# Kernel tuning notes

Measured on AMD Instinct MI355X. Metric: run time of the kernel, lower is better.

Reference implementation:

```python
import jax, jax.numpy as jnp
import numpy as np

# --- configuration constants (match init_kwargs) ---
N = 256          # num_oscillators
T = 200          # simulation steps
INTERVAL = 5     # readout_update_interval
OFFSET = 1       # spike_update_offset
DELAY = 10
D = DELAY + 1    # delay-buffer length
K_GLOBAL = 1.0   # global_coupling_strength
STEP_SIZE = 0.1
GAMMA_ATTR = 0.5 # gamma_attraction_strength
DECAY = 0.9      # membrane_decay
THRESH = 1.0
REC_SCALE = 0.1
ALPHA_FIX = 0.5  # fixed_alpha_value (fixed during training)
CLS_START = 50   # classifier_start_step
SURR_BETA = 4.0  # surrogate-gradient sharpness
NUM_CLASSES = 10


def _spike(u):
    # Heaviside forward, sigmoid surrogate backward (straight-through)
    sg = jax.nn.sigmoid(SURR_BETA * u)
    hard = (u > 0).astype(u.dtype)
    return sg + jax.lax.stop_gradient(hard - sg)


def _forward(x, theta0, W_init, omega, W_ro, W_gate, W_rec, W_fb, W_cls, b_cls):
    B = x.shape[0]
    P = W_gate.shape[1]  # num_pixels = H*W*C
    xf = x.reshape(B, -1)
    gamma0 = jnp.tanh(xf @ W_init)                 # ReadoutLayer.initialize_gamma_from_input -> [B,N]
    buf0 = jnp.tile(theta0[None], (D, 1, 1))       # theta delay buffer [D,B,N]
    zN = jnp.zeros((B, N), x.dtype)
    zP = jnp.zeros((B, P), x.dtype)
    carry0 = (theta0, gamma0, zN, zP, zP, zN, buf0)  # theta, gamma, gate, membrane, spikes, fb-activity a, buffer

    def step(carry, s):
        theta, gamma, gate, mem, spk, a, buf = carry
        # --- KuramotoLayer: dtheta_i = omega_i + K/N * sum_j (1 + W_ij*alpha) sin(th_j - th_i) + attr*gamma_i
        # top-down connectivity W_ij = a_i a_j is rank-1, so the coupling sum is computed exactly in O(N).
        sin_t = jnp.sin(theta); cos_t = jnp.cos(theta)
        S = sin_t.sum(-1, keepdims=True); C = cos_t.sum(-1, keepdims=True)
        base = cos_t * S - sin_t * C
        as_ = jnp.sum(a * sin_t, -1, keepdims=True)
        ac_ = jnp.sum(a * cos_t, -1, keepdims=True)
        weighted = ALPHA_FIX * (cos_t * a * as_ - sin_t * a * ac_)
        dtheta = omega + (K_GLOBAL / N) * (base + weighted) + GAMMA_ATTR * gamma
        theta = theta + STEP_SIZE * dtheta

        # --- ReadoutLayer.gamma_update + SinusoidalGate every INTERVAL steps
        def ro_upd(args):
            g = jnp.tanh(theta @ W_ro)
            gt = g * 0.5 * (1.0 + jnp.cos(theta - buf[0]))  # gate from delayed phase difference
            return g, gt
        gamma, gate = jax.lax.cond((s % INTERVAL) == 0, ro_upd, lambda args: args, (gamma, gate))

        # --- SNNLayer.forward_step + TopDownFeedback on offset spike-update steps
        def sp_upd(args):
            mem_, spk_, a_ = args
            cur = gate @ W_gate + REC_SCALE * (spk_ @ W_rec)
            mem_ = DECAY * mem_ * (1.0 - spk_) + cur       # leaky membrane with reset
            spk_ = _spike(mem_ - THRESH)
            a_ = jnp.tanh(spk_ @ W_fb)                     # per-oscillator feedback activity
            return mem_, spk_, a_
        m_sp = (((s - OFFSET) % INTERVAL) == 0) & (s > OFFSET)
        mem, spk, a = jax.lax.cond(m_sp, sp_upd, lambda args: args, (mem, spk, a))

        buf = jnp.concatenate([buf[1:], theta[None]], axis=0)
        return (theta, gamma, gate, mem, spk, a, buf), spk

    _, spk_hist = jax.lax.scan(step, carry0, jnp.arange(1, T + 1))
    spike_trace = jnp.transpose(spk_hist, (1, 0, 2))       # [B,T,P]
    rate = jnp.mean(spike_trace[:, CLS_START:, :], axis=1) # SNNLayer.classify: mean firing rate
    logits = rate @ W_cls + b_cls
    return logits


def setup_inputs() -> dict:
    key = jax.random.key(0)
    ks = jax.random.split(key, 10)
    B, H, W, C = 32, 32, 32, 3
    P = H * W * C
    x = jax.random.normal(ks[0], (B, H, W, C), jnp.float32)
    theta0 = jax.random.normal(ks[1], (B, N), jnp.float32)
    W_init = jax.random.normal(ks[2], (P, N), jnp.float32) / np.sqrt(P).astype(np.float32)
    omega = jax.random.normal(ks[3], (N,), jnp.float32) * 0.5
    W_ro = jax.random.normal(ks[4], (N, N), jnp.float32) / np.sqrt(N).astype(np.float32)
    W_gate = jax.random.normal(ks[5], (N, P), jnp.float32) / np.sqrt(N).astype(np.float32)
    W_rec = jax.random.normal(ks[6], (P, P), jnp.float32) / np.sqrt(P).astype(np.float32)
    W_fb = jax.random.normal(ks[7], (P, N), jnp.float32) / np.sqrt(P).astype(np.float32)
    W_cls = jax.random.normal(ks[8], (P, NUM_CLASSES), jnp.float32) / np.sqrt(P).astype(np.float32)
    b_cls = jnp.zeros((NUM_CLASSES,), jnp.float32)
    return dict(x=x, theta0=theta0, W_init=W_init, omega=omega, W_ro=W_ro,
                W_gate=W_gate, W_rec=W_rec, W_fb=W_fb, W_cls=W_cls, b_cls=b_cls)


def reference(x, theta0, W_init, omega, W_ro, W_gate, W_rec, W_fb, W_cls, b_cls):
    return _forward(x, theta0, W_init, omega, W_ro, W_gate, W_rec, W_fb, W_cls, b_cls)
```

## Files before the change

### kernel.cpp

```cpp
#include <hip/hip_runtime.h>
#include <cstdint>
#include <cstddef>

#define BB 32
#define NN 256
#define PP 3072
#define NG 192
#define RING 16

typedef unsigned short u16;

__global__ __launch_bounds__(512) void k_init(
    const float* __restrict__ x, const float* __restrict__ W_init,
    double* __restrict__ gpartI, double* __restrict__ memD,
    double* __restrict__ a_g, float* __restrict__ rate,
    u16* __restrict__ maskA, u16* __restrict__ maskB, int* __restrict__ cntG,
    int* __restrict__ cntB) {
  const int blk = blockIdx.x, tid = threadIdx.x;
  if (blk < 192) {
    const int b = blk / 6, sub = blk % 6;
    __shared__ double xl[512];
    xl[tid] = (double)x[(size_t)b * PP + sub * 512 + tid];
    __syncthreads();
    const int osc = tid & 255, kh = tid >> 8;
    const float* wp = W_init + (size_t)(sub * 512 + kh * 256) * NN + osc;
    const double* xp = xl + kh * 256;
    double a0 = 0, a1 = 0, a2 = 0, a3 = 0, a4 = 0, a5 = 0, a6 = 0, a7 = 0;
    for (int r = 0; r < 256; r += 8) {
      a0 += xp[r + 0] * (double)wp[(size_t)(r + 0) * NN];
      a1 += xp[r + 1] * (double)wp[(size_t)(r + 1) * NN];
      a2 += xp[r + 2] * (double)wp[(size_t)(r + 2) * NN];
      a3 += xp[r + 3] * (double)wp[(size_t)(r + 3) * NN];
      a4 += xp[r + 4] * (double)wp[(size_t)(r + 4) * NN];
      a5 += xp[r + 5] * (double)wp[(size_t)(r + 5) * NN];
      a6 += xp[r + 6] * (double)wp[(size_t)(r + 6) * NN];
      a7 += xp[r + 7] * (double)wp[(size_t)(r + 7) * NN];
    }
    double acc = ((a0 + a1) + (a2 + a3)) + ((a4 + a5) + (a6 + a7));
    __syncthreads();
    __shared__ double hl[256];
    if (kh) hl[osc] = acc;
    __syncthreads();
    if (!kh) gpartI[((size_t)b * 6 + sub) * 256 + osc] = acc + hl[osc];
  } else {
    const int b = blk - 192;
    for (int i = tid; i < PP; i += 512) {
      memD[(size_t)b * PP + i] = 0.0;
      rate[(size_t)b * PP + i] = 0.f;
    }
    for (int i = tid; i < NG; i += 512) {
      maskA[b * NG + i] = 0;
      maskB[b * NG + i] = 0;
    }
    for (int i = tid; i < NN; i += 512) a_g[b * NN + i] = 0.0;
    if (tid == 0) {
      cntG[b] = 0;
      cntB[b * 2 + 0] = 0;
      cntB[b * 2 + 1] = 0;
    }
  }
}

__global__ __launch_bounds__(512) void k_tg(
    double* __restrict__ ring, double* __restrict__ gamma_g,
    double* __restrict__ a_g, double* __restrict__ gateG,
    const double* __restrict__ a_part, const float* __restrict__ theta0,
    const float* __restrict__ omega, const float* __restrict__ W_ro,
    const double* __restrict__ gpartI, const float* __restrict__ W_rec,
    const u16* __restrict__ listG, const int* __restrict__ cntG,
    const int* __restrict__ cntB, double* __restrict__ recPart, int k2) {
  const int blk = blockIdx.x, tid = threadIdx.x;
  __shared__ double th[256];
  __shared__ double red[16];
  __shared__ double qpart[256];

  if (blk >= 32) {
    if (k2 >= 39) return;
    const int w = blk - 32;
    const int g = w % 192, bh = (w / 192) & 1, z = w / 384, j0 = g * 16;
    const int qd = tid & 3;
    const int h = (tid >> 2) & 7;
    const int bl = tid >> 5;
    const int b = bh * 16 + bl;
    const int beg = (z == 0) ? 0 : cntB[b * 2 + (z - 1)];
    const int end = (z == 2) ? cntG[b] : cntB[b * 2 + z];
    const u16* lst = listG + (size_t)b * PP;
    const float* wp = W_rec + j0 + 4 * qd;

    double a0 = 0, a1 = 0, a2 = 0, a3 = 0;
    int i = beg + h;
    for (; i + 32 <= end; i += 32) {
      const int r0 = lst[i], r1 = lst[i + 8], r2 = lst[i + 16],
                r3 = lst[i + 24];
      const float4 f0 = *(const float4*)(wp + (size_t)r0 * PP);
      const float4 f1 = *(const float4*)(wp + (size_t)r1 * PP);
      const float4 f2 = *(const float4*)(wp + (size_t)r2 * PP);
      const float4 f3 = *(const float4*)(wp + (size_t)r3 * PP);
      a0 += (double)f0.x; a1 += (double)f0.y; a2 += (double)f0.z; a3 += (double)f0.w;
      a0 += (double)f1.x; a1 += (double)f1.y; a2 += (double)f1.z; a3 += (double)f1.w;
      a0 += (double)f2.x; a1 += (double)f2.y; a2 += (double)f2.z; a3 += (double)f2.w;
      a0 += (double)f3.x; a1 += (double)f3.y; a2 += (double)f3.z; a3 += (double)f3.w;
    }
    for (; i < end; i += 8) {
      const float4 f = *(const float4*)(wp + (size_t)lst[i] * PP);
      a0 += (double)f.x; a1 += (double)f.y; a2 += (double)f.z; a3 += (double)f.w;
    }
    a0 += __shfl_xor(a0, 4); a0 += __shfl_xor(a0, 8); a0 += __shfl_xor(a0, 16);
    a1 += __shfl_xor(a1, 4); a1 += __shfl_xor(a1, 8); a1 += __shfl_xor(a1, 16);
    a2 += __shfl_xor(a2, 4); a2 += __shfl_xor(a2, 8); a2 += __shfl_xor(a2, 16);
    a3 += __shfl_xor(a3, 4); a3 += __shfl_xor(a3, 8); a3 += __shfl_xor(a3, 16);
    if (h == 0) {
      double* dst = recPart + ((size_t)z * BB + b) * PP + j0 + 4 * qd;
      dst[0] = a0; dst[1] = a1; dst[2] = a2; dst[3] = a3;
    }
    return;
  }

  const int b = blk;
  const int j = tid & 255, q = tid >> 8;
  const int lane = tid & 63, wid = tid >> 6;
  const int s0 = 5 * k2 + 1, s1 = 5 * k2 + 5;
  double new_a = 0.0;
  if (k2 > 0) {
    double s = 0.0;
#pragma unroll
    for (int u = 0; u < 8; ++u)
      s += a_part[((size_t)b * 16 + q * 8 + u) * NN + j];
    if (q) qpart[j] = s;
    __syncthreads();
    if (!q) new_a = tanh(s + qpart[j]);
    __syncthreads();
  }

  double t = 0.0, aj = 0.0, gm = 0.0, om = 0.0;
  if (!q) {
    om = (double)omega[j];
    if (k2 == 0) {
      double s = 0.0;
      for (int c6 = 0; c6 < 6; ++c6) s += gpartI[((size_t)b * 6 + c6) * 256 + j];
      gm = tanh(s);
      t = (double)theta0[b * NN + j];
      ring[0 * BB * NN + b * NN + j] = t;
    } else {
      t = ring[((s0 - 1) & (RING - 1)) * BB * NN + b * NN + j];
      aj = a_g[b * NN + j];
      gm = gamma_g[b * NN + j];
    }
  }

  for (int s = s0; s <= s1; ++s) {
    if (!q && k2 > 0 && s == s0 + 1) {
      aj = new_a;
      a_g[b * NN + j] = aj;
    }
    double sn = 0.0, cs = 0.0;
    if (!q) sincos(t, &sn, &cs);
    double r0 = sn, r1 = cs, r2 = aj * sn, r3 = aj * cs;
#pragma unroll
    for (int o = 32; o; o >>= 1) {
      r0 += __shfl_down(r0, o);
      r1 += __shfl_down(r1, o);
      r2 += __shfl_down(r2, o);
      r3 += __shfl_down(r3, o);
    }
    if (lane == 0 && wid < 4) {
      red[wid * 4 + 0] = r0;
      red[wid * 4 + 1] = r1;
      red[wid * 4 + 2] = r2;
      red[wid * 4 + 3] = r3;
    }
    __syncthreads();
    double S = red[0] + red[4] + red[8] + red[12];
    double C = red[1] + red[5] + red[9] + red[13];
    double AS = red[2] + red[6] + red[10] + red[14];
    double AC = red[3] + red[7] + red[11] + red[15];
    __syncthreads();
    if (!q) {
      double base = cs * S - sn * C;
      double wgt = 0.5 * (cs * aj * AS - sn * aj * AC);
      t = t + 0.1 * (om + (1.0 / 256.0) * (base + wgt) + 0.5 * gm);
      ring[(s & (RING - 1)) * BB * NN + b * NN + j] = t;
    }
  }
  if (!q) th[j] = t;
  __syncthreads();
  {
    double c0 = 0, c1 = 0, c2 = 0, c3 = 0, c4 = 0, c5 = 0, c6 = 0, c7 = 0;
    const float* wp = W_ro + j;
    const int i0 = q * 128;
    for (int i = 0; i < 128; i += 8) {
      c0 += th[i0 + i + 0] * (double)wp[(size_t)(i0 + i + 0) * NN];
      c1 += th[i0 + i + 1] * (double)wp[(size_t)(i0 + i + 1) * NN];
      c2 += th[i0 + i + 2] * (double)wp[(size_t)(i0 + i + 2) * NN];
      c3 += th[i0 + i + 3] * (double)wp[(size_t)(i0 + i + 3) * NN];
      c4 += th[i0 + i + 4] * (double)wp[(size_t)(i0 + i + 4) * NN];
      c5 += th[i0 + i + 5] * (double)wp[(size_t)(i0 + i + 5) * NN];
      c6 += th[i0 + i + 6] * (double)wp[(size_t)(i0 + i + 6) * NN];
      c7 += th[i0 + i + 7] * (double)wp[(size_t)(i0 + i + 7) * NN];
    }
    double acc = ((c0 + c1) + (c2 + c3)) + ((c4 + c5) + (c6 + c7));
    if (q) qpart[j] = acc;
    __syncthreads();
    if (!q) {
      double gnew = tanh(acc + qpart[j]);
      gamma_g[b * NN + j] = gnew;
      int sd = s1 - 11;
      if (sd < 0) sd = 0;
      double dly = ring[(sd & (RING - 1)) * BB * NN + b * NN + j];
      double gt = gnew * 0.5 * (1.0 + cos(t - dly));
      gateG[(size_t)b * 256 + j] = gt;
    }
  }
}

__global__ __launch_bounds__(512) void k_fin(
    const u16* __restrict__ mask_rd, u16* __restrict__ mask_wr,
    double* __restrict__ memD, const double* __restrict__ gateG,
    const float* __restrict__ W_gate, const double* __restrict__ recPart,
    float* __restrict__ rate, int accum) {
  __shared__ double gd[32 * 258];
  __shared__ float wt[256 * 16];
  const int g = blockIdx.x, tid = threadIdx.x, j0 = g * 16;
  for (int i = tid; i < 8192; i += 512)
    gd[(i >> 8) * 258 + (i & 255)] = gateG[(size_t)(i >> 8) * 256 + (i & 255)];
  for (int i = tid; i < 4096; i += 512)
    wt[i] = W_gate[(size_t)(i >> 4) * PP + j0 + (i & 15)];
  __syncthreads();

  const int pi = tid & 15, b = tid >> 4;
  const double* gq = gd + b * 258;
  const float* wq = wt + pi;
  double ch0, ch1, ch2, ch3;
  {
    double c[4];
#pragma unroll
    for (int cq = 0; cq < 4; ++cq) {
      const double* gc = gq + cq * 64;
      const float* wc = wq + cq * 64 * 16;
      double s0 = 0, s1 = 0, s2 = 0, s3 = 0, s4 = 0, s5 = 0, s6 = 0, s7 = 0;
      for (int k = 0; k < 64; k += 8) {
        s0 += gc[k + 0] * (double)wc[(k + 0) * 16];
        s1 += gc[k + 1] * (double)wc[(k + 1) * 16];
        s2 += gc[k + 2] * (double)wc[(k + 2) * 16];
        s3 += gc[k + 3] * (double)wc[(k + 3) * 16];
        s4 += gc[k + 4] * (double)wc[(k + 4) * 16];
        s5 += gc[k + 5] * (double)wc[(k + 5) * 16];
        s6 += gc[k + 6] * (double)wc[(k + 6) * 16];
        s7 += gc[k + 7] * (double)wc[(k + 7) * 16];
      }
      c[cq] = ((s0 + s1) + (s2 + s3)) + ((s4 + s5) + (s6 + s7));
    }
    ch0 = c[0]; ch1 = c[1]; ch2 = c[2]; ch3 = c[3];
  }
  const double vgs = (ch0 + ch1) + (ch2 + ch3);

  const int p = j0 + pi;
  const size_t idx = (size_t)b * PP + p;
  const double vrs = (recPart[idx] + recPart[(size_t)BB * PP + idx]) +
                     recPart[(size_t)2 * BB * PP + idx];
  const double cur = vgs + 0.1 * vrs;
  const double so = (double)((mask_rd[b * NG + g] >> pi) & 1);
  const double mv = 0.9 * memD[idx] * (1.0 - so) + cur;
  const double sv = (mv - 1.0 > 0.0) ? 1.0 : 0.0;
  memD[idx] = mv;
  if (accum) rate[idx] += (float)sv;
  unsigned long long bal = __ballot(sv > 0.5);
  const int lane = tid & 63;
  if ((lane & 15) == 0)
    mask_wr[b * NG + g] = (u16)((bal >> (16 * (lane >> 4))) & 0xFFFFull);
}

__global__ __launch_bounds__(256) void k_fb(
    const u16* __restrict__ spk_mask, u16* __restrict__ listG,
    int* __restrict__ cntG, int* __restrict__ cntB,
    const float* __restrict__ W_fb, double* __restrict__ a_part) {
  const int b = blockIdx.x, y = blockIdx.y, tid = threadIdx.x;
  __shared__ int pc[NG], sc[NG];
  __shared__ u16 m_l[NG];
  __shared__ u16 list_l[PP];
  if (tid < NG) {
    m_l[tid] = spk_mask[b * NG + tid];
    pc[tid] = __popc((unsigned int)m_l[tid]);
    sc[tid] = pc[tid];
  }
  __syncthreads();
  for (int d = 1; d < NG; d <<= 1) {
    int v = 0;
    if (tid < NG) v = sc[tid] + ((tid >= d) ? sc[tid - d] : 0);
    __syncthreads();
    if (tid < NG) sc[tid] = v;
    __syncthreads();
  }
  const int total = sc[NG - 1];
  if (tid < NG) {
    int off = sc[tid] - pc[tid];
    unsigned int m = m_l[tid];
    while (m) {
      int bit = __builtin_ctz(m);
      m &= m - 1;
      list_l[off++] = (u16)(tid * 16 + bit);
    }
  }
  __syncthreads();
  if (y == 0) {
    for (int i = tid; i < total; i += 256) listG[(size_t)b * PP + i] = list_l[i];
    if (tid == 0) {
      cntG[b] = total;
      cntB[b * 2 + 0] = sc[63];
      cntB[b * 2 + 1] = sc[127];
    }
  }
  const int j = tid;
  double c0 = 0, c1 = 0, c2 = 0, c3 = 0, c4 = 0, c5 = 0, c6 = 0, c7 = 0;
  int i = y;
  for (; i + 128 <= total; i += 128) {
    c0 += (double)W_fb[(size_t)list_l[i + 0] * NN + j];
    c1 += (double)W_fb[(size_t)list_l[i + 16] * NN + j];
    c2 += (double)W_fb[(size_t)list_l[i + 32] * NN + j];
    c3 += (double)W_fb[(size_t)list_l[i + 48] * NN + j];
    c4 += (double)W_fb[(size_t)list_l[i + 64] * NN + j];
    c5 += (double)W_fb[(size_t)list_l[i + 80] * NN + j];
    c6 += (double)W_fb[(size_t)list_l[i + 96] * NN + j];
    c7 += (double)W_fb[(size_t)list_l[i + 112] * NN + j];
  }
  double acc = ((c0 + c1) + (c2 + c3)) + ((c4 + c5) + (c6 + c7));
  for (; i < total; i += 16) acc += (double)W_fb[(size_t)list_l[i] * NN + j];
  a_part[((size_t)b * 16 + y) * NN + j] = acc;
}

__global__ __launch_bounds__(256) void k_cls(const float* __restrict__ rate,
                                             const float* __restrict__ Wcls,
                                             const float* __restrict__ bcls,
                                             float* __restrict__ out) {
  const int b = blockIdx.x, t = threadIdx.x;
  double acc[10];
#pragma unroll
  for (int c = 0; c < 10; ++c) acc[c] = 0.0;
  for (int p = t; p < PP; p += 256) {
    double r = (double)rate[(size_t)b * PP + p] / 30.0;
#pragma unroll
    for (int c = 0; c < 10; ++c) acc[c] += r * (double)Wcls[(size_t)p * 10 + c];
  }
  __shared__ double sh[10][256];
#pragma unroll
  for (int c = 0; c < 10; ++c) sh[c][t] = acc[c];
  __syncthreads();
  for (int off = 128; off; off >>= 1) {
    if (t < off)
#pragma unroll
      for (int c = 0; c < 10; ++c) sh[c][t] += sh[c][t + off];
    __syncthreads();
  }
  if (t < 10) out[b * 10 + t] = (float)(sh[t][0] + (double)bcls[t]);
}

extern "C" void kernel_launch(void* const* d_in, const int* in_sizes, int n_in,
                              void* d_out, int out_size, void* d_ws,
                              size_t ws_size, hipStream_t stream) {
  const float* x = (const float*)d_in[0];
  const float* theta0 = (const float*)d_in[1];
  const float* W_init = (const float*)d_in[2];
  const float* omega = (const float*)d_in[3];
  const float* W_ro = (const float*)d_in[4];
  const float* W_gate = (const float*)d_in[5];
  const float* W_rec = (const float*)d_in[6];
  const float* W_fb = (const float*)d_in[7];
  const float* W_cls = (const float*)d_in[8];
  const float* b_cls = (const float*)d_in[9];

  char* w = (char*)d_ws;
  size_t off = 0;
  auto alloc = [&](size_t sz) -> void* {
    void* p = w + off;
    off = (off + sz + 255) & ~(size_t)255;
    return p;
  };
  double* ring = (double*)alloc((size_t)RING * BB * NN * 8);
  double* gamma = (double*)alloc((size_t)BB * NN * 8);
  double* a_g = (double*)alloc((size_t)BB * NN * 8);
  double* gateG = (double*)alloc((size_t)BB * NN * 8);
  double* memD = (double*)alloc((size_t)BB * PP * 8);
  float* rate = (float*)alloc((size_t)BB * PP * 4);
  u16* maskA = (u16*)alloc((size_t)BB * NG * 2);
  u16* maskB = (u16*)alloc((size_t)BB * NG * 2);
  u16* listG = (u16*)alloc((size_t)BB * PP * 2);
  int* cntG = (int*)alloc((size_t)BB * 4);
  int* cntB = (int*)alloc((size_t)BB * 2 * 4);
  double* gpartI = (double*)alloc((size_t)BB * 6 * 256 * 8);
  double* a_part = (double*)alloc((size_t)BB * 16 * NN * 8);
  double* recPart = (double*)alloc((size_t)3 * BB * PP * 8);

  k_init<<<224, 512, 0, stream>>>(x, W_init, gpartI, memD, a_g, rate, maskA,
                                  maskB, cntG, cntB);
  k_tg<<<1184, 512, 0, stream>>>(ring, gamma, a_g, gateG, a_part, theta0,
                                 omega, W_ro, gpartI, W_rec, listG, cntG, cntB,
                                 recPart, 0);
  for (int k = 1; k < 40; ++k) {
    const u16* mrd = (k & 1) ? maskA : maskB;
    u16* mwr = (k & 1) ? maskB : maskA;
    k_fin<<<192, 512, 0, stream>>>(mrd, mwr, memD, gateG, W_gate, recPart,
                                   rate, (k >= 10) ? 1 : 0);
    k_fb<<<dim3(32, 16), 256, 0, stream>>>(mwr, listG, cntG, cntB, W_fb,
                                           a_part);
    k_tg<<<1184, 512, 0, stream>>>(ring, gamma, a_g, gateG, a_part, theta0,
                                   omega, W_ro, gpartI, W_rec, listG, cntG,
                                   cntB, recPart, k);
  }
  k_cls<<<32, 256, 0, stream>>>(rate, W_cls, b_cls, (float*)d_out);
}
```

Baseline: 1.974 ms.

## Fuse feedback kernel into theta/gamma kernel and read spike masks directly

Removes the separate k_fb launch per iteration. The 32 theta blocks of k_tg now build the compacted spike list from the bitmask in shared memory and compute the W_fb feedback themselves with 2-way splitting instead of 16. The W_rec blocks iterate set bits of the mask directly instead of reading a global list and counts. This saves one launch and global round-trips per step, at the cost of less parallelism for the feedback sum, which is now serialized into the 32 critical-path blocks, and more shared memory in k_tg.

```diff
diff --git a/kernel.cpp b/kernel.cpp
--- a/kernel.cpp
+++ b/kernel.cpp
@@ -14,8 +14,7 @@
     const float* __restrict__ x, const float* __restrict__ W_init,
     double* __restrict__ gpartI, double* __restrict__ memD,
     double* __restrict__ a_g, float* __restrict__ rate,
-    u16* __restrict__ maskA, u16* __restrict__ maskB, int* __restrict__ cntG,
-    int* __restrict__ cntB) {
+    u16* __restrict__ maskA, u16* __restrict__ maskB) {
   const int blk = blockIdx.x, tid = threadIdx.x;
   if (blk < 192) {
     const int b = blk / 6, sub = blk % 6;
@@ -53,26 +52,23 @@
       maskB[b * NG + i] = 0;
     }
     for (int i = tid; i < NN; i += 512) a_g[b * NN + i] = 0.0;
-    if (tid == 0) {
-      cntG[b] = 0;
-      cntB[b * 2 + 0] = 0;
-      cntB[b * 2 + 1] = 0;
-    }
   }
 }
 
 __global__ __launch_bounds__(512) void k_tg(
     double* __restrict__ ring, double* __restrict__ gamma_g,
     double* __restrict__ a_g, double* __restrict__ gateG,
-    const double* __restrict__ a_part, const float* __restrict__ theta0,
+    const u16* __restrict__ mask_cur, const float* __restrict__ theta0,
     const float* __restrict__ omega, const float* __restrict__ W_ro,
-    const double* __restrict__ gpartI, const float* __restrict__ W_rec,
-    const u16* __restrict__ listG, const int* __restrict__ cntG,
-    const int* __restrict__ cntB, double* __restrict__ recPart, int k2) {
+    const float* __restrict__ W_fb, const double* __restrict__ gpartI,
+    const float* __restrict__ W_rec, double* __restrict__ recPart, int k2) {
   const int blk = blockIdx.x, tid = threadIdx.x;
   __shared__ double th[256];
   __shared__ double red[16];
   __shared__ double qpart[256];
+  __shared__ int pc[NG], sc[NG];
+  __shared__ u16 m_l[NG];
+  __shared__ u16 list_l[PP];
 
   if (blk >= 32) {
     if (k2 >= 39) return;
@@ -82,29 +78,33 @@
     const int h = (tid >> 2) & 7;
     const int bl = tid >> 5;
     const int b = bh * 16 + bl;
-    const int beg = (z == 0) ? 0 : cntB[b * 2 + (z - 1)];
-    const int end = (z == 2) ? cntG[b] : cntB[b * 2 + z];
-    const u16* lst = listG + (size_t)b * PP;
+    const u16* mk = mask_cur + b * NG;
     const float* wp = W_rec + j0 + 4 * qd;
-
-    double a0 = 0, a1 = 0, a2 = 0, a3 = 0;
-    int i = beg + h;
-    for (; i + 32 <= end; i += 32) {
-      const int r0 = lst[i], r1 = lst[i + 8], r2 = lst[i + 16],
-                r3 = lst[i + 24];
-      const float4 f0 = *(const float4*)(wp + (size_t)r0 * PP);
-      const float4 f1 = *(const float4*)(wp + (size_t)r1 * PP);
-      const float4 f2 = *(const float4*)(wp + (size_t)r2 * PP);
-      const float4 f3 = *(const float4*)(wp + (size_t)r3 * PP);
-      a0 += (double)f0.x; a1 += (double)f0.y; a2 += (double)f0.z; a3 += (double)f0.w;
-      a0 += (double)f1.x; a1 += (double)f1.y; a2 += (double)f1.z; a3 += (double)f1.w;
-      a0 += (double)f2.x; a1 += (double)f2.y; a2 += (double)f2.z; a3 += (double)f2.w;
-      a0 += (double)f3.x; a1 += (double)f3.y; a2 += (double)f3.z; a3 += (double)f3.w;
-    }
-    for (; i < end; i += 8) {
-      const float4 f = *(const float4*)(wp + (size_t)lst[i] * PP);
-      a0 += (double)f.x; a1 += (double)f.y; a2 += (double)f.z; a3 += (double)f.w;
-    }
+    const int gb = 64 * z + h;
+
+    double x0 = 0, y0 = 0, u0 = 0, v0 = 0, x1 = 0, y1 = 0, u1 = 0, v1 = 0,
+           x2 = 0, y2 = 0, u2 = 0, v2 = 0, x3 = 0, y3 = 0, u3 = 0, v3 = 0;
+#define CHG(X, Y, U, V, G)                                          \
+  {                                                                 \
+    unsigned int m = (unsigned int)mk[G];                           \
+    const int rb = (G) * 16;                                        \
+    while (m) {                                                     \
+      const int bit = __builtin_ctz(m);                             \
+      m &= m - 1;                                                   \
+      const float4 f = *(const float4*)(wp + (size_t)(rb + bit) * PP); \
+      X += (double)f.x; Y += (double)f.y;                           \
+      U += (double)f.z; V += (double)f.w;                           \
+    }                                                               \
+  }
+    CHG(x0, y0, u0, v0, gb + 0);  CHG(x0, y0, u0, v0, gb + 32);
+    CHG(x1, y1, u1, v1, gb + 8);  CHG(x1, y1, u1, v1, gb + 40);
+    CHG(x2, y2, u2, v2, gb + 16); CHG(x2, y2, u2, v2, gb + 48);
+    CHG(x3, y3, u3, v3, gb + 24); CHG(x3, y3, u3, v3, gb + 56);
+#undef CHG
+    double a0 = (x0 + x1) + (x2 + x3);
+    double a1 = (y0 + y1) + (y2 + y3);
+    double a2 = (u0 + u1) + (u2 + u3);
+    double a3 = (v0 + v1) + (v2 + v3);
     a0 += __shfl_xor(a0, 4); a0 += __shfl_xor(a0, 8); a0 += __shfl_xor(a0, 16);
     a1 += __shfl_xor(a1, 4); a1 += __shfl_xor(a1, 8); a1 += __shfl_xor(a1, 16);
     a2 += __shfl_xor(a2, 4); a2 += __shfl_xor(a2, 8); a2 += __shfl_xor(a2, 16);
@@ -121,15 +121,52 @@
   const int lane = tid & 63, wid = tid >> 6;
   const int s0 = 5 * k2 + 1, s1 = 5 * k2 + 5;
   double new_a = 0.0;
+
   if (k2 > 0) {
-    double s = 0.0;
-#pragma unroll
-    for (int u = 0; u < 8; ++u)
-      s += a_part[((size_t)b * 16 + q * 8 + u) * NN + j];
-    if (q) qpart[j] = s;
-    __syncthreads();
-    if (!q) new_a = tanh(s + qpart[j]);
-    __syncthreads();
+    if (tid < NG) {
+      m_l[tid] = mask_cur[b * NG + tid];
+      pc[tid] = __popc((unsigned int)m_l[tid]);
+      sc[tid] = pc[tid];
+    }
+    __syncthreads();
+    for (int d = 1; d < NG; d <<= 1) {
+      int v = 0;
+      if (tid < NG) v = sc[tid] + ((tid >= d) ? sc[tid - d] : 0);
+      __syncthreads();
+      if (tid < NG) sc[tid] = v;
+      __syncthreads();
+    }
+    const int total = sc[NG - 1];
+    if (tid < NG) {
+      int off = sc[tid] - pc[tid];
+      unsigned int m = m_l[tid];
+      while (m) {
+        int bit = __builtin_ctz(m);
+        m &= m - 1;
+        list_l[off++] = (u16)(tid * 16 + bit);
+      }
+    }
+    __syncthreads();
+    {
+      double c0 = 0, c1 = 0, c2 = 0, c3 = 0, c4 = 0, c5 = 0, c6 = 0, c7 = 0;
+      int i = q;
+      for (; i + 16 <= total; i += 16) {
+        c0 += (double)W_fb[(size_t)list_l[i + 0] * NN + j];
+        c1 += (double)W_fb[(size_t)list_l[i + 2] * NN + j];
+        c2 += (double)W_fb[(size_t)list_l[i + 4] * NN + j];
+        c3 += (double)W_fb[(size_t)list_l[i + 6] * NN + j];
+        c4 += (double)W_fb[(size_t)list_l[i + 8] * NN + j];
+        c5 += (double)W_fb[(size_t)list_l[i + 10] * NN + j];
+        c6 += (double)W_fb[(size_t)list_l[i + 12] * NN + j];
+        c7 += (double)W_fb[(size_t)list_l[i + 14] * NN + j];
+      }
+      double acc = ((c0 + c1) + (c2 + c3)) + ((c4 + c5) + (c6 + c7));
+      for (; i < total; i += 2) acc += (double)W_fb[(size_t)list_l[i] * NN + j];
+      if (q) qpart[j] = acc;
+      __syncthreads();
+      if (!q) new_a = tanh(acc + qpart[j]);
+      __syncthreads();
+    }
   }
 
   double t = 0.0, aj = 0.0, gm = 0.0, om = 0.0;
@@ -230,29 +267,25 @@
   const int pi = tid & 15, b = tid >> 4;
   const double* gq = gd + b * 258;
   const float* wq = wt + pi;
-  double ch0, ch1, ch2, ch3;
-  {
-    double c[4];
-#pragma unroll
-    for (int cq = 0; cq < 4; ++cq) {
-      const double* gc = gq + cq * 64;
-      const float* wc = wq + cq * 64 * 16;
-      double s0 = 0, s1 = 0, s2 = 0, s3 = 0, s4 = 0, s5 = 0, s6 = 0, s7 = 0;
-      for (int k = 0; k < 64; k += 8) {
-        s0 += gc[k + 0] * (double)wc[(k + 0) * 16];
-        s1 += gc[k + 1] * (double)wc[(k + 1) * 16];
-        s2 += gc[k + 2] * (double)wc[(k + 2) * 16];
-        s3 += gc[k + 3] * (double)wc[(k + 3) * 16];
-        s4 += gc[k + 4] * (double)wc[(k + 4) * 16];
-        s5 += gc[k + 5] * (double)wc[(k + 5) * 16];
-        s6 += gc[k + 6] * (double)wc[(k + 6) * 16];
-        s7 += gc[k + 7] * (double)wc[(k + 7) * 16];
-      }
-      c[cq] = ((s0 + s1) + (s2 + s3)) + ((s4 + s5) + (s6 + s7));
-    }
-    ch0 = c[0]; ch1 = c[1]; ch2 = c[2]; ch3 = c[3];
-  }
-  const double vgs = (ch0 + ch1) + (ch2 + ch3);
+  double ch[4];
+#pragma unroll
+  for (int cq = 0; cq < 4; ++cq) {
+    const double* gc = gq + cq * 64;
+    const float* wc = wq + cq * 64 * 16;
+    double s0 = 0, s1 = 0, s2 = 0, s3 = 0, s4 = 0, s5 = 0, s6 = 0, s7 = 0;
+    for (int k = 0; k < 64; k += 8) {
+      s0 += gc[k + 0] * (double)wc[(k + 0) * 16];
+      s1 += gc[k + 1] * (double)wc[(k + 1) * 16];
+      s2 += gc[k + 2] * (double)wc[(k + 2) * 16];
+      s3 += gc[k + 3] * (double)wc[(k + 3) * 16];
+      s4 += gc[k + 4] * (double)wc[(k + 4) * 16];
+      s5 += gc[k + 5] * (double)wc[(k + 5) * 16];
+      s6 += gc[k + 6] * (double)wc[(k + 6) * 16];
+      s7 += gc[k + 7] * (double)wc[(k + 7) * 16];
+    }
+    ch[cq] = ((s0 + s1) + (s2 + s3)) + ((s4 + s5) + (s6 + s7));
+  }
+  const double vgs = (ch[0] + ch[1]) + (ch[2] + ch[3]);
 
   const int p = j0 + pi;
   const size_t idx = (size_t)b * PP + p;
@@ -268,64 +301,6 @@
   const int lane = tid & 63;
   if ((lane & 15) == 0)
     mask_wr[b * NG + g] = (u16)((bal >> (16 * (lane >> 4))) & 0xFFFFull);
-}
-
-__global__ __launch_bounds__(256) void k_fb(
-    const u16* __restrict__ spk_mask, u16* __restrict__ listG,
-    int* __restrict__ cntG, int* __restrict__ cntB,
-    const float* __restrict__ W_fb, double* __restrict__ a_part) {
-  const int b = blockIdx.x, y = blockIdx.y, tid = threadIdx.x;
-  __shared__ int pc[NG], sc[NG];
-  __shared__ u16 m_l[NG];
-  __shared__ u16 list_l[PP];
-  if (tid < NG) {
-    m_l[tid] = spk_mask[b * NG + tid];
-    pc[tid] = __popc((unsigned int)m_l[tid]);
-    sc[tid] = pc[tid];
-  }
-  __syncthreads();
-  for (int d = 1; d < NG; d <<= 1) {
-    int v = 0;
-    if (tid < NG) v = sc[tid] + ((tid >= d) ? sc[tid - d] : 0);
-    __syncthreads();
-    if (tid < NG) sc[tid] = v;
-    __syncthreads();
-  }
-  const int total = sc[NG - 1];
-  if (tid < NG) {
-    int off = sc[tid] - pc[tid];
-    unsigned int m = m_l[tid];
-    while (m) {
-      int bit = __builtin_ctz(m);
-      m &= m - 1;
-      list_l[off++] = (u16)(tid * 16 + bit);
-    }
-  }
-  __syncthreads();
-  if (y == 0) {
-    for (int i = tid; i < total; i += 256) listG[(size_t)b * PP + i] = list_l[i];
-    if (tid == 0) {
-      cntG[b] = total;
-      cntB[b * 2 + 0] = sc[63];
-      cntB[b * 2 + 1] = sc[127];
-    }
-  }
-  const int j = tid;
-  double c0 = 0, c1 = 0, c2 = 0, c3 = 0, c4 = 0, c5 = 0, c6 = 0, c7 = 0;
-  int i = y;
-  for (; i + 128 <= total; i += 128) {
-    c0 += (double)W_fb[(size_t)list_l[i + 0] * NN + j];
-    c1 += (double)W_fb[(size_t)list_l[i + 16] * NN + j];
-    c2 += (double)W_fb[(size_t)list_l[i + 32] * NN + j];
-    c3 += (double)W_fb[(size_t)list_l[i + 48] * NN + j];
-    c4 += (double)W_fb[(size_t)list_l[i + 64] * NN + j];
-    c5 += (double)W_fb[(size_t)list_l[i + 80] * NN + j];
-    c6 += (double)W_fb[(size_t)list_l[i + 96] * NN + j];
-    c7 += (double)W_fb[(size_t)list_l[i + 112] * NN + j];
-  }
-  double acc = ((c0 + c1) + (c2 + c3)) + ((c4 + c5) + (c6 + c7));
-  for (; i < total; i += 16) acc += (double)W_fb[(size_t)list_l[i] * NN + j];
-  a_part[((size_t)b * 16 + y) * NN + j] = acc;
 }
 
 __global__ __launch_bounds__(256) void k_cls(const float* __restrict__ rate,
@@ -383,28 +358,20 @@
   float* rate = (float*)alloc((size_t)BB * PP * 4);
   u16* maskA = (u16*)alloc((size_t)BB * NG * 2);
   u16* maskB = (u16*)alloc((size_t)BB * NG * 2);
-  u16* listG = (u16*)alloc((size_t)BB * PP * 2);
-  int* cntG = (int*)alloc((size_t)BB * 4);
-  int* cntB = (int*)alloc((size_t)BB * 2 * 4);
   double* gpartI = (double*)alloc((size_t)BB * 6 * 256 * 8);
-  double* a_part = (double*)alloc((size_t)BB * 16 * NN * 8);
   double* recPart = (double*)alloc((size_t)3 * BB * PP * 8);
 
   k_init<<<224, 512, 0, stream>>>(x, W_init, gpartI, memD, a_g, rate, maskA,
-                                  maskB, cntG, cntB);
-  k_tg<<<1184, 512, 0, stream>>>(ring, gamma, a_g, gateG, a_part, theta0,
-                                 omega, W_ro, gpartI, W_rec, listG, cntG, cntB,
-                                 recPart, 0);
+                                  maskB);
+  k_tg<<<1184, 512, 0, stream>>>(ring, gamma, a_g, gateG, maskA, theta0, omega,
+                                 W_ro, W_fb, gpartI, W_rec, recPart, 0);
   for (int k = 1; k < 40; ++k) {
     const u16* mrd = (k & 1) ? maskA : maskB;
     u16* mwr = (k & 1) ? maskB : maskA;
     k_fin<<<192, 512, 0, stream>>>(mrd, mwr, memD, gateG, W_gate, recPart,
                                    rate, (k >= 10) ? 1 : 0);
-    k_fb<<<dim3(32, 16), 256, 0, stream>>>(mwr, listG, cntG, cntB, W_fb,
-                                           a_part);
-    k_tg<<<1184, 512, 0, stream>>>(ring, gamma, a_g, gateG, a_part, theta0,
-                                   omega, W_ro, gpartI, W_rec, listG, cntG,
-                                   cntB, recPart, k);
+    k_tg<<<1184, 512, 0, stream>>>(ring, gamma, a_g, gateG, mwr, theta0, omega,
+                                   W_ro, W_fb, gpartI, W_rec, recPart, k);
   }
   k_cls<<<32, 256, 0, stream>>>(rate, W_cls, b_cls, (float*)d_out);
 }
```

New measurement: 2.647 ms. 1.34x slower.
